# Kernel tuning notes

Measured on AMD Instinct MI355X. Metric: run time of the kernel, lower is better.

Reference implementation:

```python
import jax, jax.numpy as jnp
import numpy as np

B, SQ, SK, D, DV = 8, 2048, 2048, 256, 256


def setup_inputs() -> dict:
    key = jax.random.key(0)
    kq, kk, kv, kw = jax.random.split(key, 4)
    queries = jax.random.normal(kq, (B, SQ, D), dtype=jnp.float32)
    keys = jax.random.normal(kk, (B, SK, D), dtype=jnp.float32)
    values = jax.random.normal(kv, (B, SK, DV), dtype=jnp.float32)
    # nn.Linear(query_dim + value_dim, query_dim): weight (out,in) in torch; store as (in,out)
    W = jax.random.normal(kw, (D + DV, D), dtype=jnp.float32) * (1.0 / np.sqrt(D + DV))
    b = jnp.zeros((D,), dtype=jnp.float32)
    return {"queries": queries, "keys": keys, "values": values, "W": W, "b": b}


def reference(queries, keys, values, W, b):
    scale = 1.0 / jnp.sqrt(jnp.asarray(keys.shape[-1], queries.dtype))
    # scores: (B, Sq, Sk)
    scores = jnp.einsum('bqd,bkd->bqk', queries, keys) * scale
    attn = jax.nn.softmax(scores, axis=-1)
    context = jnp.einsum('bqk,bkv->bqv', attn, values)  # (B, Sq, Dv)
    combined = jnp.concatenate([context, queries], axis=-1)  # (B, Sq, Dv+D)
    return combined @ W + b
```

## Files before the change

### kernel.cpp

```cpp
#include <hip/hip_runtime.h>
#include <stdint.h>

#define BATCH 8
#define SEQ   2048
#define DIM   256
#define NKV   64
#define KT8   8192
#define NWT   16
#define WT    16384
#define VOFF  ((size_t)BATCH * NKV * KT8)
#define WOFF  (VOFF + (size_t)BATCH * NKV * KT8)
#define C1    0.090215498f
#define THRRAW 88.6766f

typedef __attribute__((ext_vector_type(8))) short bf16x8;
typedef __attribute__((ext_vector_type(4))) float f32x4;
typedef __attribute__((ext_vector_type(4))) unsigned int u32x4;

__device__ __forceinline__ unsigned short f2bf(float x) {
    unsigned u = __float_as_uint(x);
    unsigned r = u + 0x7fffu + ((u >> 16) & 1u);
    return (unsigned short)(r >> 16);
}
__device__ __forceinline__ unsigned pack2(float a, float b) {
    return (unsigned)f2bf(a) | ((unsigned)f2bf(b) << 16);
}
__device__ __forceinline__ float exp2_fast(float x) {
    float r;
    asm("v_exp_f32 %0, %1" : "=v"(r) : "v"(x));
    return r;
}
__device__ __forceinline__ unsigned pk8x4(float a, float b, float c, float d) {
    unsigned u = __builtin_amdgcn_cvt_pk_fp8_f32(a, b, 0, false);
    return __builtin_amdgcn_cvt_pk_fp8_f32(c, d, u, true);
}
__device__ __forceinline__ long long mk64(unsigned lo, unsigned hi) {
    return (long long)(((unsigned long long)hi << 32) | lo);
}
__device__ __forceinline__ unsigned bperm(int srclane, unsigned v) {
    return (unsigned)__builtin_amdgcn_ds_bpermute(srclane * 4, (int)v);
}

__global__ void prep_frags(const float* __restrict__ K, const float* __restrict__ V,
                           const float* __restrict__ W, uint8_t* __restrict__ ws) {
    const int bid = blockIdx.x, tid = threadIdx.x;
    const int lane = tid & 63, fb = tid >> 6, g = lane >> 4, nn = lane & 15;
    if (bid < BATCH * NKV) {
        const float* src = K + (size_t)bid * 32 * DIM;
        uint8_t* dst = ws + (size_t)bid * KT8;
#pragma unroll
        for (int p = 0; p < 2; ++p) {
            int pr = p * 4 + fb, t2 = pr >> 2, kk2 = pr & 3;
            const float* rp = src + (size_t)(t2 * 16 + nn) * DIM + kk2 * 64 + g * 8;
            float4 a  = *(const float4*)(rp);
            float4 a2 = *(const float4*)(rp + 4);
            float4 c  = *(const float4*)(rp + 32);
            float4 c2 = *(const float4*)(rp + 36);
            u32x4 u = {pk8x4(a.x, a.y, a.z, a.w), pk8x4(a2.x, a2.y, a2.z, a2.w),
                       pk8x4(c.x, c.y, c.z, c.w), pk8x4(c2.x, c2.y, c2.z, c2.w)};
            *(u32x4*)(dst + pr * 1024 + lane * 16) = u;
        }
    } else if (bid < 2 * BATCH * NKV) {
        const int id = bid - BATCH * NKV;
        const float* src = V + (size_t)id * 32 * DIM;
        uint8_t* dst = ws + VOFF + (size_t)id * KT8;
#pragma unroll
        for (int p = 0; p < 2; ++p) {
            int pr = p * 4 + fb;
            float v0[8], v1[8];
#pragma unroll
            for (int j = 0; j < 8; ++j) {
                v0[j] = src[(size_t)(g * 8 + j) * DIM + pr * 32 + nn];
                v1[j] = src[(size_t)(g * 8 + j) * DIM + pr * 32 + 16 + nn];
            }
            u32x4 u = {pk8x4(v0[0], v0[1], v0[2], v0[3]), pk8x4(v0[4], v0[5], v0[6], v0[7]),
                       pk8x4(v1[0], v1[1], v1[2], v1[3]), pk8x4(v1[4], v1[5], v1[6], v1[7])};
            *(u32x4*)(dst + pr * 1024 + lane * 16) = u;
        }
    } else {
        const int wt = bid - 2 * BATCH * NKV;
        const float* src = W + (size_t)wt * 32 * DIM;
        uint8_t* dst = ws + WOFF + (size_t)wt * WT;
#pragma unroll
        for (int p = 0; p < 4; ++p) {
            int d = p * 4 + fb;
            float v[8];
#pragma unroll
            for (int j = 0; j < 8; ++j)
                v[j] = src[(size_t)(g * 8 + j) * DIM + d * 16 + nn];
            u32x4 u = {pack2(v[0], v[1]), pack2(v[2], v[3]),
                       pack2(v[4], v[5]), pack2(v[6], v[7])};
            *(u32x4*)(dst + d * 1024 + lane * 16) = u;
        }
    }
}

#define SMEM_BYTES 50816

__launch_bounds__(256, 2)
__global__ void attn_main(const float* __restrict__ Q, const float* __restrict__ bias,
                          const uint8_t* __restrict__ ws, float* __restrict__ out) {
    __shared__ __align__(16) uint8_t smem[SMEM_BYTES];
    float* cbuf = (float*)smem;
    uint8_t* cbn = smem + 32768;
    float* mws = (float*)(smem + 49664);
    float* lws = (float*)(smem + 50176);
    float* lgb = (float*)(smem + 50688);

    const int tid = threadIdx.x;
    const int wid = tid >> 6, lane = tid & 63, g = lane >> 4, nn = lane & 15;
    const int b = blockIdx.x & 7, qg = blockIdx.x >> 3;
    const int q0 = qg * 32;

    {
        f32x4 z = {0.f, 0.f, 0.f, 0.f};
        float* p = cbuf + tid * 32;
#pragma unroll
        for (int i = 0; i < 8; ++i) *(f32x4*)(p + i * 4) = z;
    }

    const float* qbase = Q + ((size_t)b * SEQ + q0 + nn) * DIM + g * 8;
    long long qp[2][8];
#pragma unroll
    for (int rt = 0; rt < 2; ++rt)
#pragma unroll
        for (int t8 = 0; t8 < 8; ++t8) {
            const float* rp = qbase + (size_t)rt * 16 * DIM + t8 * 32;
            float4 a = *(const float4*)(rp);
            float4 c = *(const float4*)(rp + 4);
            qp[rt][t8] = mk64(pk8x4(a.x, a.y, a.z, a.w), pk8x4(c.x, c.y, c.z, c.w));
        }

    f32x4 ctx[2][16];
#pragma unroll
    for (int rt = 0; rt < 2; ++rt)
#pragma unroll
        for (int d = 0; d < 16; ++d) ctx[rt][d] = (f32x4){0.f, 0.f, 0.f, 0.f};
    float m[2] = {-3e38f, -3e38f}, mc[2] = {0.f, 0.f}, l[2] = {0.f, 0.f};

    const uint8_t* kws = ws + ((size_t)b * NKV + wid * 16) * KT8 + lane * 16;
    const uint8_t* vws = ws + VOFF + ((size_t)b * NKV + wid * 16) * KT8 + lane * 16;

    for (int t = 0; t < 16; ++t) {
        const uint8_t* kf = kws + (size_t)t * KT8;
        const uint8_t* vf = vws + (size_t)t * KT8;
        u32x4 kp[8];
#pragma unroll
        for (int i = 0; i < 8; ++i) kp[i] = *(const u32x4*)(kf + i * 1024);
        f32x4 s[2][2];
#pragma unroll
        for (int rt = 0; rt < 2; ++rt) { s[rt][0] = (f32x4){0.f,0.f,0.f,0.f}; s[rt][1] = s[rt][0]; }
#pragma unroll
        for (int kk = 0; kk < 8; ++kk) {
            int i = kk >> 1, h = kk & 1;
            long long ka = mk64(kp[i][2 * h], kp[i][2 * h + 1]);
            long long kb2 = mk64(kp[4 + i][2 * h], kp[4 + i][2 * h + 1]);
#pragma unroll
            for (int rt = 0; rt < 2; ++rt) {
                s[rt][0] = __builtin_amdgcn_mfma_f32_16x16x32_fp8_fp8(ka,  qp[rt][kk], s[rt][0], 0, 0, 0);
                s[rt][1] = __builtin_amdgcn_mfma_f32_16x16x32_fp8_fp8(kb2, qp[rt][kk], s[rt][1], 0, 0, 0);
            }
        }
        float smax[2];
        int need = 0;
#pragma unroll
        for (int rt = 0; rt < 2; ++rt) {
            smax[rt] = fmaxf(fmaxf(fmaxf(s[rt][0][0], s[rt][0][1]), fmaxf(s[rt][0][2], s[rt][0][3])),
                             fmaxf(fmaxf(s[rt][1][0], s[rt][1][1]), fmaxf(s[rt][1][2], s[rt][1][3])));
            need |= (smax[rt] > m[rt] + THRRAW);
        }
        if (__any(need)) {
#pragma unroll
            for (int rt = 0; rt < 2; ++rt) {
                float v = smax[rt];
                v = fmaxf(v, __shfl_xor(v, 16));
                v = fmaxf(v, __shfl_xor(v, 32));
                float mn = fmaxf(m[rt], v);
                float sc0 = exp2_fast((m[rt] - mn) * C1);
                m[rt] = mn; mc[rt] = mn * C1; l[rt] *= sc0;
                float scr[4];
#pragma unroll
                for (int r = 0; r < 4; ++r)
                    scr[r] = __uint_as_float(bperm(4 * g + r, __float_as_uint(sc0)));
#pragma unroll
                for (int d = 0; d < 16; ++d)
#pragma unroll
                    for (int r = 0; r < 4; ++r) ctx[rt][d][r] *= scr[r];
            }
        }
        unsigned pkA[2], pkB[2];
#pragma unroll
        for (int rt = 0; rt < 2; ++rt) {
            float p0[4], p1[4];
#pragma unroll
            for (int r = 0; r < 4; ++r) {
                p0[r] = exp2_fast(__builtin_fmaf(s[rt][0][r], C1, -mc[rt]));
                p1[r] = exp2_fast(__builtin_fmaf(s[rt][1][r], C1, -mc[rt]));
                l[rt] += p0[r] + p1[r];
            }
            pkA[rt] = pk8x4(p0[0], p0[1], p0[2], p0[3]);
            pkB[rt] = pk8x4(p1[0], p1[1], p1[2], p1[3]);
        }
        u32x4 vp[8];
#pragma unroll
        for (int i = 0; i < 8; ++i) vp[i] = *(const u32x4*)(vf + i * 1024);
        long long A[2];
        {
            int alo = ((2 * g) & 3) * 16 + nn;
#pragma unroll
            for (int rt = 0; rt < 2; ++rt) {
                unsigned b00 = bperm(alo, pkA[rt]),      b01 = bperm(alo, pkB[rt]);
                unsigned b10 = bperm(alo + 16, pkA[rt]), b11 = bperm(alo + 16, pkB[rt]);
                A[rt] = mk64((g < 2) ? b00 : b01, (g < 2) ? b10 : b11);
            }
        }
#pragma unroll
        for (int i = 0; i < 4; ++i) {
            long long v0 = mk64(vp[i][0], vp[i][1]), v1 = mk64(vp[i][2], vp[i][3]);
#pragma unroll
            for (int rt = 0; rt < 2; ++rt) {
                ctx[rt][2 * i]     = __builtin_amdgcn_mfma_f32_16x16x32_fp8_fp8(A[rt], v0, ctx[rt][2 * i], 0, 0, 0);
                ctx[rt][2 * i + 1] = __builtin_amdgcn_mfma_f32_16x16x32_fp8_fp8(A[rt], v1, ctx[rt][2 * i + 1], 0, 0, 0);
            }
        }
#pragma unroll
        for (int i = 0; i < 4; ++i) {
            long long v0 = mk64(vp[4 + i][0], vp[4 + i][1]), v1 = mk64(vp[4 + i][2], vp[4 + i][3]);
#pragma unroll
            for (int rt = 0; rt < 2; ++rt) {
                ctx[rt][8 + 2 * i]     = __builtin_amdgcn_mfma_f32_16x16x32_fp8_fp8(A[rt], v0, ctx[rt][8 + 2 * i], 0, 0, 0);
                ctx[rt][8 + 2 * i + 1] = __builtin_amdgcn_mfma_f32_16x16x32_fp8_fp8(A[rt], v1, ctx[rt][8 + 2 * i + 1], 0, 0, 0);
            }
        }
    }

#pragma unroll
    for (int rt = 0; rt < 2; ++rt) {
        l[rt] += __shfl_xor(l[rt], 16);
        l[rt] += __shfl_xor(l[rt], 32);
    }

    if (lane < 16) {
#pragma unroll
        for (int rt = 0; rt < 2; ++rt) {
            mws[wid * 32 + rt * 16 + nn] = m[rt];
            lws[wid * 32 + rt * 16 + nn] = l[rt];
        }
    }
    __syncthreads();
    float sc[2][4];
#pragma unroll
    for (int rt = 0; rt < 2; ++rt)
#pragma unroll
        for (int r = 0; r < 4; ++r) {
            int row = rt * 16 + g * 4 + r;
            float m0 = mws[row], m1 = mws[32 + row], m2 = mws[64 + row], m3 = mws[96 + row];
            float mg = fmaxf(fmaxf(m0, m1), fmaxf(m2, m3));
            float lg = lws[row]      * exp2_fast((m0 - mg) * C1)
                     + lws[32 + row] * exp2_fast((m1 - mg) * C1)
                     + lws[64 + row] * exp2_fast((m2 - mg) * C1)
                     + lws[96 + row] * exp2_fast((m3 - mg) * C1);
            sc[rt][r] = exp2_fast((mws[wid * 32 + row] - mg) * C1);
            if (wid == 0 && nn == 0) lgb[row] = lg;
        }
    for (int w = 0; w < 4; ++w) {
        if (wid == w) {
#pragma unroll
            for (int rt = 0; rt < 2; ++rt)
#pragma unroll
                for (int d = 0; d < 16; ++d)
#pragma unroll
                    for (int r = 0; r < 4; ++r) {
                        float* p = cbuf + (size_t)(rt * 16 + g * 4 + r) * 256 + d * 16 + nn;
                        *p += ctx[rt][d][r] * sc[rt][r];
                    }
        }
        __syncthreads();
    }
    {
        int row = tid >> 3, c0 = (tid & 7) * 32;
        float il = 1.0f / lgb[row];
        const float* src = cbuf + (size_t)row * 256 + c0;
        uint8_t* dp = cbn + (size_t)row * 528 + c0 * 2;
#pragma unroll
        for (int i = 0; i < 4; ++i) {
            f32x4 a = *(const f32x4*)(src + i * 8);
            f32x4 c = *(const f32x4*)(src + i * 8 + 4);
            u32x4 u = {pack2(a[0] * il, a[1] * il), pack2(a[2] * il, a[3] * il),
                       pack2(c[0] * il, c[1] * il), pack2(c[2] * il, c[3] * il)};
            *(u32x4*)(dp + i * 16) = u;
        }
    }
    __syncthreads();

    bf16x8 qe[2][8];
#pragma unroll
    for (int rt = 0; rt < 2; ++rt)
#pragma unroll
        for (int t8 = 0; t8 < 8; ++t8) {
            const float* rp = qbase + (size_t)rt * 16 * DIM + t8 * 32;
            float4 a = *(const float4*)(rp);
            float4 c = *(const float4*)(rp + 4);
            union { bf16x8 v; unsigned u[4]; } tmp;
            tmp.u[0] = pack2(a.x, a.y); tmp.u[1] = pack2(a.z, a.w);
            tmp.u[2] = pack2(c.x, c.y); tmp.u[3] = pack2(c.z, c.w);
            qe[rt][t8] = tmp.v;
        }
    f32x4 oacc[2][4];
#pragma unroll
    for (int rt = 0; rt < 2; ++rt)
#pragma unroll
        for (int dd = 0; dd < 4; ++dd) oacc[rt][dd] = (f32x4){0.f, 0.f, 0.f, 0.f};
    const uint8_t* wws = ws + WOFF + lane * 16;
    for (int wt = 0; wt < NWT; ++wt) {
        bf16x8 af[2];
#pragma unroll
        for (int rt = 0; rt < 2; ++rt) {
            if (wt < 8) af[rt] = *(const bf16x8*)(cbn + (size_t)(rt * 16 + nn) * 528 + wt * 64 + g * 16);
            else        af[rt] = qe[rt][wt - 8];
        }
#pragma unroll
        for (int dd = 0; dd < 4; ++dd) {
            bf16x8 wf = *(const bf16x8*)(wws + (size_t)(wt * 16 + wid * 4 + dd) * 1024);
#pragma unroll
            for (int rt = 0; rt < 2; ++rt)
                oacc[rt][dd] = __builtin_amdgcn_mfma_f32_16x16x32_bf16(af[rt], wf, oacc[rt][dd], 0, 0, 0);
        }
    }
#pragma unroll
    for (int rt = 0; rt < 2; ++rt) {
        float* obase = out + ((size_t)b * SEQ + q0 + rt * 16) * DIM + wid * 64;
#pragma unroll
        for (int dd = 0; dd < 4; ++dd) {
            float bv = bias[wid * 64 + dd * 16 + nn];
#pragma unroll
            for (int r = 0; r < 4; ++r)
                obase[(size_t)(g * 4 + r) * DIM + dd * 16 + nn] = oacc[rt][dd][r] + bv;
        }
    }
}

extern "C" void kernel_launch(void* const* d_in, const int* in_sizes, int n_in,
                              void* d_out, int out_size, void* d_ws, size_t ws_size,
                              hipStream_t stream) {
    const float* Q    = (const float*)d_in[0];
    const float* K    = (const float*)d_in[1];
    const float* V    = (const float*)d_in[2];
    const float* W    = (const float*)d_in[3];
    const float* bias = (const float*)d_in[4];
    float* out = (float*)d_out;
    uint8_t* ws = (uint8_t*)d_ws;
    prep_frags<<<2 * BATCH * NKV + NWT, 256, 0, stream>>>(K, V, W, ws);
    attn_main<<<BATCH * SEQ / 32, 256, 0, stream>>>(Q, bias, ws, out);
}
```

Before: 71.26 us.

## Prefetch next K tile with ping-pong registers and use permlane swaps for P

Restructures the KV loop into a two-step unrolled body. The next K tile is loaded into a second register buffer while the current tile's softmax and PV work runs, so global-load latency overlaps compute. It replaces the four ds_bpermute shuffles that built the P operand with v_permlane32/16 swap instructions. It also raises wave priority around the MFMA blocks and adds a scheduling barrier. The extra K register buffer raises register pressure under the 2-blocks-per-SM launch bound, and the final iteration makes one redundant reload of the last tile.

```diff
diff --git a/kernel.cpp b/kernel.cpp
--- a/kernel.cpp
+++ b/kernel.cpp
@@ -97,6 +97,89 @@
 
 #define SMEM_BYTES 50816
 
+__device__ __forceinline__ void kv_step(
+    const u32x4 (&kp)[8], u32x4 (&kpn)[8],
+    const uint8_t* __restrict__ kfn, const uint8_t* __restrict__ vf,
+    const long long (&qp)[2][8], f32x4 (&ctx)[2][16],
+    float (&m)[2], float (&mc)[2], float (&l)[2], const int g, const int nn) {
+    f32x4 s[2][2];
+    s[0][0] = (f32x4){0.f, 0.f, 0.f, 0.f};
+    s[0][1] = s[0][0]; s[1][0] = s[0][0]; s[1][1] = s[0][0];
+    __builtin_amdgcn_s_setprio(1);
+#pragma unroll
+    for (int kk = 0; kk < 8; ++kk) {
+        int i = kk >> 1, h = kk & 1;
+        long long ka  = mk64(kp[i][2 * h], kp[i][2 * h + 1]);
+        long long kb2 = mk64(kp[4 + i][2 * h], kp[4 + i][2 * h + 1]);
+#pragma unroll
+        for (int rt = 0; rt < 2; ++rt) {
+            s[rt][0] = __builtin_amdgcn_mfma_f32_16x16x32_fp8_fp8(ka,  qp[rt][kk], s[rt][0], 0, 0, 0);
+            s[rt][1] = __builtin_amdgcn_mfma_f32_16x16x32_fp8_fp8(kb2, qp[rt][kk], s[rt][1], 0, 0, 0);
+        }
+    }
+    __builtin_amdgcn_s_setprio(0);
+    __builtin_amdgcn_sched_barrier(0);
+#pragma unroll
+    for (int i = 0; i < 8; ++i) kpn[i] = *(const u32x4*)(kfn + i * 1024);
+    u32x4 vp[8];
+#pragma unroll
+    for (int i = 0; i < 8; ++i) vp[i] = *(const u32x4*)(vf + i * 1024);
+    float smax[2];
+    int need = 0;
+#pragma unroll
+    for (int rt = 0; rt < 2; ++rt) {
+        smax[rt] = fmaxf(fmaxf(fmaxf(s[rt][0][0], s[rt][0][1]), fmaxf(s[rt][0][2], s[rt][0][3])),
+                         fmaxf(fmaxf(s[rt][1][0], s[rt][1][1]), fmaxf(s[rt][1][2], s[rt][1][3])));
+        need |= (smax[rt] > m[rt] + THRRAW);
+    }
+    if (__any(need)) {
+#pragma unroll
+        for (int rt = 0; rt < 2; ++rt) {
+            float v = smax[rt];
+            v = fmaxf(v, __shfl_xor(v, 16));
+            v = fmaxf(v, __shfl_xor(v, 32));
+            float mn = fmaxf(m[rt], v);
+            float sc0 = exp2_fast((m[rt] - mn) * C1);
+            m[rt] = mn; mc[rt] = mn * C1; l[rt] *= sc0;
+            float scr[4];
+#pragma unroll
+            for (int r = 0; r < 4; ++r)
+                scr[r] = __uint_as_float(bperm(4 * g + r, __float_as_uint(sc0)));
+#pragma unroll
+            for (int d = 0; d < 16; ++d)
+#pragma unroll
+                for (int r = 0; r < 4; ++r) ctx[rt][d][r] *= scr[r];
+        }
+    }
+    long long A[2];
+#pragma unroll
+    for (int rt = 0; rt < 2; ++rt) {
+        float p0[4], p1[4];
+#pragma unroll
+        for (int r = 0; r < 4; ++r) {
+            p0[r] = exp2_fast(__builtin_fmaf(s[rt][0][r], C1, -mc[rt]));
+            p1[r] = exp2_fast(__builtin_fmaf(s[rt][1][r], C1, -mc[rt]));
+            l[rt] += p0[r] + p1[r];
+        }
+        unsigned a  = pk8x4(p0[0], p0[1], p0[2], p0[3]);
+        unsigned b2 = pk8x4(p1[0], p1[1], p1[2], p1[3]);
+        asm("v_permlane32_swap_b32 %0, %1" : "+v"(a), "+v"(b2));
+        asm("v_permlane16_swap_b32 %0, %1" : "+v"(a), "+v"(b2));
+        A[rt] = mk64(a, b2);
+    }
+    __builtin_amdgcn_s_setprio(1);
+#pragma unroll
+    for (int i = 0; i < 8; ++i) {
+        long long v0 = mk64(vp[i][0], vp[i][1]), v1 = mk64(vp[i][2], vp[i][3]);
+#pragma unroll
+        for (int rt = 0; rt < 2; ++rt) {
+            ctx[rt][2 * i]     = __builtin_amdgcn_mfma_f32_16x16x32_fp8_fp8(A[rt], v0, ctx[rt][2 * i], 0, 0, 0);
+            ctx[rt][2 * i + 1] = __builtin_amdgcn_mfma_f32_16x16x32_fp8_fp8(A[rt], v1, ctx[rt][2 * i + 1], 0, 0, 0);
+        }
+    }
+    __builtin_amdgcn_s_setprio(0);
+}
+
 __launch_bounds__(256, 2)
 __global__ void attn_main(const float* __restrict__ Q, const float* __restrict__ bias,
                           const uint8_t* __restrict__ ws, float* __restrict__ out) {
@@ -141,97 +224,16 @@
     const uint8_t* kws = ws + ((size_t)b * NKV + wid * 16) * KT8 + lane * 16;
     const uint8_t* vws = ws + VOFF + ((size_t)b * NKV + wid * 16) * KT8 + lane * 16;
 
-    for (int t = 0; t < 16; ++t) {
-        const uint8_t* kf = kws + (size_t)t * KT8;
-        const uint8_t* vf = vws + (size_t)t * KT8;
-        u32x4 kp[8];
-#pragma unroll
-        for (int i = 0; i < 8; ++i) kp[i] = *(const u32x4*)(kf + i * 1024);
-        f32x4 s[2][2];
-#pragma unroll
-        for (int rt = 0; rt < 2; ++rt) { s[rt][0] = (f32x4){0.f,0.f,0.f,0.f}; s[rt][1] = s[rt][0]; }
-#pragma unroll
-        for (int kk = 0; kk < 8; ++kk) {
-            int i = kk >> 1, h = kk & 1;
-            long long ka = mk64(kp[i][2 * h], kp[i][2 * h + 1]);
-            long long kb2 = mk64(kp[4 + i][2 * h], kp[4 + i][2 * h + 1]);
-#pragma unroll
-            for (int rt = 0; rt < 2; ++rt) {
-                s[rt][0] = __builtin_amdgcn_mfma_f32_16x16x32_fp8_fp8(ka,  qp[rt][kk], s[rt][0], 0, 0, 0);
-                s[rt][1] = __builtin_amdgcn_mfma_f32_16x16x32_fp8_fp8(kb2, qp[rt][kk], s[rt][1], 0, 0, 0);
-            }
-        }
-        float smax[2];
-        int need = 0;
-#pragma unroll
-        for (int rt = 0; rt < 2; ++rt) {
-            smax[rt] = fmaxf(fmaxf(fmaxf(s[rt][0][0], s[rt][0][1]), fmaxf(s[rt][0][2], s[rt][0][3])),
-                             fmaxf(fmaxf(s[rt][1][0], s[rt][1][1]), fmaxf(s[rt][1][2], s[rt][1][3])));
-            need |= (smax[rt] > m[rt] + THRRAW);
-        }
-        if (__any(need)) {
-#pragma unroll
-            for (int rt = 0; rt < 2; ++rt) {
-                float v = smax[rt];
-                v = fmaxf(v, __shfl_xor(v, 16));
-                v = fmaxf(v, __shfl_xor(v, 32));
-                float mn = fmaxf(m[rt], v);
-                float sc0 = exp2_fast((m[rt] - mn) * C1);
-                m[rt] = mn; mc[rt] = mn * C1; l[rt] *= sc0;
-                float scr[4];
-#pragma unroll
-                for (int r = 0; r < 4; ++r)
-                    scr[r] = __uint_as_float(bperm(4 * g + r, __float_as_uint(sc0)));
-#pragma unroll
-                for (int d = 0; d < 16; ++d)
-#pragma unroll
-                    for (int r = 0; r < 4; ++r) ctx[rt][d][r] *= scr[r];
-            }
-        }
-        unsigned pkA[2], pkB[2];
-#pragma unroll
-        for (int rt = 0; rt < 2; ++rt) {
-            float p0[4], p1[4];
-#pragma unroll
-            for (int r = 0; r < 4; ++r) {
-                p0[r] = exp2_fast(__builtin_fmaf(s[rt][0][r], C1, -mc[rt]));
-                p1[r] = exp2_fast(__builtin_fmaf(s[rt][1][r], C1, -mc[rt]));
-                l[rt] += p0[r] + p1[r];
-            }
-            pkA[rt] = pk8x4(p0[0], p0[1], p0[2], p0[3]);
-            pkB[rt] = pk8x4(p1[0], p1[1], p1[2], p1[3]);
-        }
-        u32x4 vp[8];
-#pragma unroll
-        for (int i = 0; i < 8; ++i) vp[i] = *(const u32x4*)(vf + i * 1024);
-        long long A[2];
-        {
-            int alo = ((2 * g) & 3) * 16 + nn;
-#pragma unroll
-            for (int rt = 0; rt < 2; ++rt) {
-                unsigned b00 = bperm(alo, pkA[rt]),      b01 = bperm(alo, pkB[rt]);
-                unsigned b10 = bperm(alo + 16, pkA[rt]), b11 = bperm(alo + 16, pkB[rt]);
-                A[rt] = mk64((g < 2) ? b00 : b01, (g < 2) ? b10 : b11);
-            }
-        }
-#pragma unroll
-        for (int i = 0; i < 4; ++i) {
-            long long v0 = mk64(vp[i][0], vp[i][1]), v1 = mk64(vp[i][2], vp[i][3]);
-#pragma unroll
-            for (int rt = 0; rt < 2; ++rt) {
-                ctx[rt][2 * i]     = __builtin_amdgcn_mfma_f32_16x16x32_fp8_fp8(A[rt], v0, ctx[rt][2 * i], 0, 0, 0);
-                ctx[rt][2 * i + 1] = __builtin_amdgcn_mfma_f32_16x16x32_fp8_fp8(A[rt], v1, ctx[rt][2 * i + 1], 0, 0, 0);
-            }
-        }
-#pragma unroll
-        for (int i = 0; i < 4; ++i) {
-            long long v0 = mk64(vp[4 + i][0], vp[4 + i][1]), v1 = mk64(vp[4 + i][2], vp[4 + i][3]);
-#pragma unroll
-            for (int rt = 0; rt < 2; ++rt) {
-                ctx[rt][8 + 2 * i]     = __builtin_amdgcn_mfma_f32_16x16x32_fp8_fp8(A[rt], v0, ctx[rt][8 + 2 * i], 0, 0, 0);
-                ctx[rt][8 + 2 * i + 1] = __builtin_amdgcn_mfma_f32_16x16x32_fp8_fp8(A[rt], v1, ctx[rt][8 + 2 * i + 1], 0, 0, 0);
-            }
-        }
+    u32x4 kpA[8], kpB[8];
+#pragma unroll
+    for (int i = 0; i < 8; ++i) kpA[i] = *(const u32x4*)(kws + i * 1024);
+
+    for (int t = 0; t < 16; t += 2) {
+        kv_step(kpA, kpB, kws + (size_t)(t + 1) * KT8, vws + (size_t)t * KT8,
+                qp, ctx, m, mc, l, g, nn);
+        int tn = (t + 2 < 16) ? t + 2 : 15;
+        kv_step(kpB, kpA, kws + (size_t)tn * KT8, vws + (size_t)(t + 1) * KT8,
+                qp, ctx, m, mc, l, g, nn);
     }
 
 #pragma unroll
```

Result: slower. 73.05 us (+2.5%).
